# Performance work log

Measured on AMD Instinct MI355X. Metric: run time of the kernel, lower is better.

The kernel has to match this reference:

```python
import jax, jax.numpy as jnp
import numpy as np

RES = 320
B = 32

def make_trajectory():
    # Faithful to get_init_trajectory_full: grid points (i,j), zeroed inside the
    # skip bands (i in [140,170] OR j in [120,160]), then shifted by -res/2.
    I, J = np.meshgrid(np.arange(RES), np.arange(RES), indexing='ij')
    pts = np.stack([I, J], axis=-1).astype(np.float32)
    skip = ((I >= 140) & (I <= 170)) | ((J >= 120) & (J <= 160))
    pts[skip] = 0.0
    pts = pts.reshape(-1, 2) - 0.5 * RES
    return jnp.asarray(pts)

def setup_inputs():
    key = jax.random.key(0)
    k_space_input = jax.random.normal(key, (B, 1, RES, RES, 2), dtype=jnp.float32)
    trajectory = make_trajectory()
    return {"k_space_input": k_space_input, "trajectory": trajectory}

def _forward(k_space_input, trajectory):
    H = W = RES
    b = k_space_input.shape[0]
    # [B,1,H,W,2] -> permute(0,1,4,2,3).squeeze(1) -> [B,2,H,W]
    ksp = jnp.transpose(k_space_input[:, 0], (0, 3, 1, 2))
    c = ksp[:, 0] + 1j * ksp[:, 1]                       # [B,H,W] complex k-space

    # --- bilinear grid-sample at trajectory points (zero padding, align_corners=False) ---
    g = trajectory * (2.0 / W)                           # normalize [-res/2,res/2] -> [-1,1]
    x = ((g[:, 0] + 1.0) * W - 1.0) * 0.5                # pixel x (width)
    y = ((g[:, 1] + 1.0) * H - 1.0) * 0.5                # pixel y (height)
    x0f = jnp.floor(x); y0f = jnp.floor(y)
    fx = x - x0f; fy = y - y0f
    x0 = x0f.astype(jnp.int32); y0 = y0f.astype(jnp.int32)
    corners = ((x0,     y0,     (1 - fx) * (1 - fy)),
               (x0 + 1, y0,     fx       * (1 - fy)),
               (x0,     y0 + 1, (1 - fx) * fy),
               (x0 + 1, y0 + 1, fx       * fy))

    def gather(ix, iy):
        valid = (ix >= 0) & (ix < W) & (iy >= 0) & (iy < H)
        v = c[:, jnp.clip(iy, 0, H - 1), jnp.clip(ix, 0, W - 1)]   # [B,N]
        return jnp.where(valid[None, :], v, 0.0)

    sub = sum(gather(ix, iy) * w[None, :] for ix, iy, w in corners)  # [B,N] sampled k-space

    # --- NUFFT adjoint: bilinear gridding (adjoint scatter-add) + centered inverse FFT ---
    grid = jnp.zeros((b, H * W), dtype=sub.dtype)
    for ix, iy, w in corners:
        valid = (ix >= 0) & (ix < W) & (iy >= 0) & (iy < H)
        idx = jnp.clip(iy, 0, H - 1) * W + jnp.clip(ix, 0, W - 1)
        grid = grid.at[:, idx].add(sub * jnp.where(valid, w, 0.0)[None, :])
    kgrid = grid.reshape(b, H, W)
    img = jnp.fft.fftshift(
        jnp.fft.ifft2(jnp.fft.ifftshift(kgrid, axes=(-2, -1)), axes=(-2, -1)),
        axes=(-2, -1)) * (H * W)                          # adjoint DFT = N * centered ifft
    out = jnp.stack([img.real, img.imag], axis=1)         # [B,2,H,W]
    return out[:, None]                                   # unsqueeze(1) -> [B,1,2,H,W]

def reference(k_space_input, trajectory):
    return _forward(k_space_input, trajectory)
```

## Files before the change

### kernel.cpp

```cpp
#include <hip/hip_runtime.h>

#define RES 320
#define CELLS (RES * RES)
#define MDIM 640
#define NCOLS 10240
#define UF 192

#define DEGC 1360.625f

typedef __attribute__((ext_vector_type(8))) short short8;
typedef __attribute__((ext_vector_type(4))) float f32x4;

static __device__ __forceinline__ short f2bf(float f) {
    unsigned u = __builtin_bit_cast(unsigned, f);
    unsigned r = (u + 0x7fffu + ((u >> 16) & 1u)) >> 16;
    return (short)r;
}

#define GLD16(g, l) __builtin_amdgcn_global_load_lds(                        \
    (const __attribute__((address_space(1))) void*)(g),                      \
    (__attribute__((address_space(3))) void*)(l), 16, 0, 0)

__global__ __launch_bounds__(256) void stencil_mt(const float2* __restrict__ ksp,
                                                  short* __restrict__ B1t,
                                                  float* __restrict__ g00,
                                                  short* __restrict__ Ff) {
    __shared__ float2 Ls[32][33];
    int tid = threadIdx.x;

    if (blockIdx.x < 240) {
        int idx0 = (blockIdx.x * 256 + tid) * 2;
        int row = idx0 / RES, y0 = idx0 % RES;
        int isfi = row >= UF;
        int u = row - UF * isfi;
        unsigned pk = 0;
        if (u <= 160) {
#pragma unroll
            for (int h = 0; h < 2; h++) {
                int y = y0 + h;
                int rr = (u * y) % RES;
                float s, c;
                sincospif((float)rr * (2.0f / RES), &s, &c);
                float sign = ((u + y) & 1) ? -1.0f : 1.0f;
                float val = isfi ? sign * s : sign * c;
                pk |= ((unsigned)(unsigned short)f2bf(val)) << (16 * h);
            }
        }
        *(unsigned*)(Ff + idx0) = pk;
    }

    int d = blockIdx.x;
    int xcd = d & 7, r = d >> 3;
    int bb = xcd * 4 + r / 100;
    int tile = r % 100;
    int tx0 = (tile % 10) * 32, ty0 = (tile / 10) * 32;
    int xl = tid & 31, yq = tid >> 5;
    int xc = tid >> 3, yg = tid & 7;
    const float2* kb = ksp + (size_t)bb * CELLS;

    int x = tx0 + xl;
    int ax = (x < 140 || x > 170) ? 1 : 0;
    int axp = (x <= 318 && (x + 1 < 140 || x + 1 > 170)) ? 1 : 0;
    float Axs[3] = {(x >= 1) ? (float)ax : 0.f, (float)(ax + axp), (float)axp};

#pragma unroll
    for (int rr = 0; rr < 4; rr++) {
        int yl = yq + 8 * rr;
        int y = ty0 + yl;
        int by = (y < 120 || y > 160) ? 1 : 0;
        int byp = (y <= 318 && (y + 1 < 120 || y + 1 > 160)) ? 1 : 0;
        float Bys[3] = {(y >= 1) ? (float)by : 0.f, (float)(by + byp), (float)byp};

        float re = 0.f, im = 0.f;
#pragma unroll
        for (int s = 0; s < 9; s++) {
            int dy = s / 3 - 1, dx = s % 3 - 1;
            float w = 0.0625f * Axs[s % 3] * Bys[s / 3];
            int yn = min(max(y + dy, 0), RES - 1);
            int xn = min(max(x + dx, 0), RES - 1);
            float2 v = kb[yn * RES + xn];
            re = fmaf(w, v.x, re);
            im = fmaf(w, v.y, im);
        }
        if ((y | x) == 0) {
            float2 v0 = kb[0];
            re = fmaf(DEGC, v0.x, re);
            im = fmaf(DEGC, v0.y, im);
            g00[2 * bb] = re;
            g00[2 * bb + 1] = im;
            re = 0.f;
            im = 0.f;
        }
        Ls[yl][xl] = make_float2(re, im);
    }
    __syncthreads();
    float2 v0 = Ls[yg * 4 + 0][xc], v1 = Ls[yg * 4 + 1][xc];
    float2 v2 = Ls[yg * 4 + 2][xc], v3 = Ls[yg * 4 + 3][xc];
    uint2 pr, pi;
    pr.x = (unsigned short)f2bf(v0.x) | ((unsigned)(unsigned short)f2bf(v1.x) << 16);
    pr.y = (unsigned short)f2bf(v2.x) | ((unsigned)(unsigned short)f2bf(v3.x) << 16);
    pi.x = (unsigned short)f2bf(v0.y) | ((unsigned)(unsigned short)f2bf(v1.y) << 16);
    pi.y = (unsigned short)f2bf(v2.y) | ((unsigned)(unsigned short)f2bf(v3.y) << 16);
    size_t rowbase = ((size_t)bb * RES + tx0 + xc) * MDIM;
    *(uint2*)(B1t + rowbase + ty0 + yg * 4) = pr;
    *(uint2*)(B1t + rowbase + RES + ty0 + yg * 4) = pi;
}

__global__ __launch_bounds__(256) void gemm1(const short* __restrict__ Ff,
                                             const short* __restrict__ B1t,
                                             short* __restrict__ C1) {
    __shared__ __align__(16) union {
        struct { short At[2][128 * 32]; short Bt[2][128 * 32]; } s;
        float Q[2][64 * 64];
    } sm;
    int tid = threadIdx.x;
    int lane = tid & 63, wave = tid >> 6;
    int wr = wave >> 1, wc = wave & 1;
    int n0c = blockIdx.x * 64;
    int u0 = blockIdx.y * 64;
    int q = lane >> 4, tl = lane & 15;
    int row4 = tid >> 2, ko = (tid & 3) * 8;
    f32x4 acc[4][4];
#pragma unroll
    for (int i = 0; i < 4; i++)
#pragma unroll
        for (int j = 0; j < 4; j++) acc[i][j] = {0.f, 0.f, 0.f, 0.f};

#define STG1(buf, k0)                                                        \
    {                                                                        \
        GLD16(Ff + (size_t)(u0 + row4) * RES + (k0) + ko,                    \
              sm.s.At[buf] + (size_t)(wave * 64) * 8);                       \
        GLD16(Ff + (size_t)(UF + u0 + row4) * RES + (k0) + ko,               \
              sm.s.At[buf] + (size_t)(256 + wave * 64) * 8);                 \
        GLD16(B1t + (size_t)(n0c + row4) * MDIM + (k0) + ko,                 \
              sm.s.Bt[buf] + (size_t)(wave * 64) * 8);                       \
        GLD16(B1t + (size_t)(n0c + row4) * MDIM + RES + (k0) + ko,           \
              sm.s.Bt[buf] + (size_t)(256 + wave * 64) * 8);                 \
    }

    STG1(0, 0);
    __syncthreads();
    int cur = 0;
    for (int kt = 0; kt < 10; kt++) {
        if (kt < 9) STG1(cur ^ 1, (kt + 1) * 32);
        short8 a[4], bf[4];
#pragma unroll
        for (int i = 0; i < 4; i++)
            a[i] = *(const short8*)&sm.s.At[cur][(wr * 64 + i * 16 + tl) * 32 + q * 8];
#pragma unroll
        for (int j = 0; j < 4; j++)
            bf[j] = *(const short8*)&sm.s.Bt[cur][(wc * 64 + j * 16 + tl) * 32 + q * 8];
#pragma unroll
        for (int i = 0; i < 4; i++)
#pragma unroll
            for (int j = 0; j < 4; j++)
                acc[i][j] = __builtin_amdgcn_mfma_f32_16x16x32_bf16(a[i], bf[j], acc[i][j], 0, 0, 0);
        __syncthreads();
        cur ^= 1;
    }
    if (wave == 1 || wave == 3) {
        float* dst = sm.Q[wave >> 1];
#pragma unroll
        for (int i = 0; i < 4; i++)
#pragma unroll
            for (int j = 0; j < 4; j++)
#pragma unroll
                for (int t = 0; t < 4; t++)
                    dst[(i * 16 + q * 4 + t) * 64 + j * 16 + tl] = acc[i][j][t];
    }
    __syncthreads();
    if (wave == 0) {
#pragma unroll
        for (int i = 0; i < 4; i++)
#pragma unroll
            for (int j = 0; j < 4; j++)
#pragma unroll
                for (int t = 0; t < 4; t++) {
                    int r = i * 16 + q * 4 + t, cl = j * 16 + tl;
                    int u = u0 + r, col = n0c + cl;
                    float q22 = sm.Q[1][r * 64 + cl];
                    if (u <= 160)
                        C1[(size_t)u * NCOLS + col] = f2bf(acc[i][j][t] - q22);
                    if (u >= 1 && u <= 159)
                        C1[(size_t)(RES - u) * NCOLS + col] = f2bf(acc[i][j][t] + q22);
                }
    } else if (wave == 2) {
#pragma unroll
        for (int i = 0; i < 4; i++)
#pragma unroll
            for (int j = 0; j < 4; j++)
#pragma unroll
                for (int t = 0; t < 4; t++) {
                    int r = i * 16 + q * 4 + t, cl = j * 16 + tl;
                    int u = u0 + r, col = n0c + cl;
                    float q12 = sm.Q[0][r * 64 + cl];
                    if (u <= 160)
                        C1[(size_t)(RES + u) * NCOLS + col] = f2bf(q12 + acc[i][j][t]);
                    if (u >= 1 && u <= 159)
                        C1[(size_t)(2 * RES - u) * NCOLS + col] = f2bf(q12 - acc[i][j][t]);
                }
    }
}

__global__ __launch_bounds__(256) void gemm2(const short* __restrict__ C1,
                                             const short* __restrict__ Ff,
                                             const float* __restrict__ g00,
                                             float* __restrict__ out) {
    __shared__ __align__(16) union {
        struct { short At[2][128 * 32]; short Bt[2][128 * 32]; } s;
        float Q[2][64 * 64];
    } sm;
    int tid = threadIdx.x;
    int lane = tid & 63, wave = tid >> 6;
    int wr = wave >> 1, wc = wave & 1;
    int bu0 = blockIdx.x * 64;
    int n0 = blockIdx.y * 64;
    int q = lane >> 4, tl = lane & 15;
    int row4 = tid >> 2, ko = (tid & 3) * 8;
    f32x4 acc[4][4];
#pragma unroll
    for (int i = 0; i < 4; i++)
#pragma unroll
        for (int j = 0; j < 4; j++) acc[i][j] = {0.f, 0.f, 0.f, 0.f};

    int gr_s = bu0 + row4;
    unsigned bb_s = (unsigned)gr_s / 320u;
    int m_s = gr_s - (int)bb_s * 320;

#define STG2(buf, k0)                                                        \
    {                                                                        \
        GLD16(C1 + (size_t)m_s * NCOLS + bb_s * RES + (k0) + ko,             \
              sm.s.At[buf] + (size_t)(wave * 64) * 8);                       \
        GLD16(C1 + (size_t)(RES + m_s) * NCOLS + bb_s * RES + (k0) + ko,     \
              sm.s.At[buf] + (size_t)(256 + wave * 64) * 8);                 \
        GLD16(Ff + (size_t)(n0 + row4) * RES + (k0) + ko,                    \
              sm.s.Bt[buf] + (size_t)(wave * 64) * 8);                       \
        GLD16(Ff + (size_t)(UF + n0 + row4) * RES + (k0) + ko,               \
              sm.s.Bt[buf] + (size_t)(256 + wave * 64) * 8);                 \
    }

    STG2(0, 0);
    __syncthreads();
    int cur = 0;
    for (int kt = 0; kt < 10; kt++) {
        if (kt < 9) STG2(cur ^ 1, (kt + 1) * 32);
        short8 a[4], bf[4];
#pragma unroll
        for (int i = 0; i < 4; i++)
            a[i] = *(const short8*)&sm.s.At[cur][(wr * 64 + i * 16 + tl) * 32 + q * 8];
#pragma unroll
        for (int j = 0; j < 4; j++)
            bf[j] = *(const short8*)&sm.s.Bt[cur][(wc * 64 + j * 16 + tl) * 32 + q * 8];
#pragma unroll
        for (int i = 0; i < 4; i++)
#pragma unroll
            for (int j = 0; j < 4; j++)
                acc[i][j] = __builtin_amdgcn_mfma_f32_16x16x32_bf16(a[i], bf[j], acc[i][j], 0, 0, 0);
        __syncthreads();
        cur ^= 1;
    }
    if (wave == 1 || wave == 3) {
        float* dst = sm.Q[wave >> 1];
#pragma unroll
        for (int i = 0; i < 4; i++)
#pragma unroll
            for (int j = 0; j < 4; j++)
#pragma unroll
                for (int t = 0; t < 4; t++)
                    dst[(i * 16 + q * 4 + t) * 64 + j * 16 + tl] = acc[i][j][t];
    }
    __syncthreads();
    if (wave == 0) {
#pragma unroll
        for (int i = 0; i < 4; i++)
#pragma unroll
            for (int j = 0; j < 4; j++)
#pragma unroll
                for (int t = 0; t < 4; t++) {
                    int r = i * 16 + q * 4 + t, cl = j * 16 + tl;
                    int gr = bu0 + r;
                    unsigned bb = (unsigned)gr / 320u;
                    int m = gr - (int)bb * 320;
                    int np = n0 + cl;
                    float q2 = sm.Q[1][r * 64 + cl];
                    float g = g00[2 * bb];
                    float sgn = ((m + np) & 1) ? -1.0f : 1.0f;
                    size_t rowb = ((size_t)bb * 2 * RES + m) * RES;
                    if (np <= 160)
                        out[rowb + np] = (acc[i][j][t] - q2) + sgn * g;
                    if (np >= 1 && np <= 159)
                        out[rowb + (RES - np)] = (acc[i][j][t] + q2) + sgn * g;
                }
    } else if (wave == 2) {
#pragma unroll
        for (int i = 0; i < 4; i++)
#pragma unroll
            for (int j = 0; j < 4; j++)
#pragma unroll
                for (int t = 0; t < 4; t++) {
                    int r = i * 16 + q * 4 + t, cl = j * 16 + tl;
                    int gr = bu0 + r;
                    unsigned bb = (unsigned)gr / 320u;
                    int m = gr - (int)bb * 320;
                    int np = n0 + cl;
                    float q3 = sm.Q[0][r * 64 + cl];
                    float g = g00[2 * bb + 1];
                    float sgn = ((m + np) & 1) ? -1.0f : 1.0f;
                    size_t rowb = (((size_t)bb * 2 + 1) * RES + m) * RES;
                    if (np <= 160)
                        out[rowb + np] = (q3 + acc[i][j][t]) + sgn * g;
                    if (np >= 1 && np <= 159)
                        out[rowb + (RES - np)] = (acc[i][j][t] - q3) + sgn * g;
                }
    }
}

extern "C" void kernel_launch(void* const* d_in, const int* in_sizes, int n_in,
                              void* d_out, int out_size, void* d_ws, size_t ws_size,
                              hipStream_t stream) {
    const float* ksp = (const float*)d_in[0];

    short* Ff = (short*)d_ws;
    short* B1t = Ff + (size_t)2 * UF * RES;
    short* C1 = B1t + (size_t)NCOLS * MDIM;
    float* g00 = (float*)(C1 + (size_t)MDIM * NCOLS);

    stencil_mt<<<3200, 256, 0, stream>>>((const float2*)ksp, B1t, g00, Ff);
    gemm1<<<dim3(160, 3), 256, 0, stream>>>(Ff, B1t, C1);
    gemm2<<<dim3(160, 3), 256, 0, stream>>>(C1, Ff, g00, (float*)d_out);
}
```

Baseline: 114.5 us.

## Fold separable stencil into DFT matrices and read raw k-space in gemm1

The 3x3 separable gridding stencil is folded algebraically into the DFT twiddle matrices (FB along one axis, FA along the other), so the separate stencil pass and its B1t intermediate disappear. gemm1 now loads raw float2 k-space directly, converting it to bf16 in registers and writing it to padded LDS, and overlaps those loads with the MFMA work. The DC correction is computed in the gemm2 epilogue straight from the input. This cuts a full read/write pass over the batch, but gemm1 now uses register-staged loads instead of direct-to-LDS loads, and the stencil weights are rounded to bf16 inside the matrices.

```diff
diff --git a/kernel.cpp b/kernel.cpp
--- a/kernel.cpp
+++ b/kernel.cpp
@@ -21,140 +21,111 @@
     (const __attribute__((address_space(1))) void*)(g),                      \
     (__attribute__((address_space(3))) void*)(l), 16, 0, 0)
 
-__global__ __launch_bounds__(256) void stencil_mt(const float2* __restrict__ ksp,
-                                                  short* __restrict__ B1t,
-                                                  float* __restrict__ g00,
-                                                  short* __restrict__ Ff) {
-    __shared__ float2 Ls[32][33];
-    int tid = threadIdx.x;
-
-    if (blockIdx.x < 240) {
-        int idx0 = (blockIdx.x * 256 + tid) * 2;
-        int row = idx0 / RES, y0 = idx0 % RES;
-        int isfi = row >= UF;
-        int u = row - UF * isfi;
-        unsigned pk = 0;
-        if (u <= 160) {
-#pragma unroll
-            for (int h = 0; h < 2; h++) {
-                int y = y0 + h;
-                int rr = (u * y) % RES;
-                float s, c;
-                sincospif((float)rr * (2.0f / RES), &s, &c);
-                float sign = ((u + y) & 1) ? -1.0f : 1.0f;
-                float val = isfi ? sign * s : sign * c;
-                pk |= ((unsigned)(unsigned short)f2bf(val)) << (16 * h);
+__global__ __launch_bounds__(256) void gen_fafb(short* __restrict__ FBf,
+                                                short* __restrict__ FAf) {
+    int idx = blockIdx.x * 256 + threadIdx.x;
+    int mat = idx / (2 * UF * RES);
+    int r = idx - mat * (2 * UF * RES);
+    int row = r / RES, c = r % RES;
+    int plane = row >= UF;
+    int n = row - UF * plane;
+    float vr = 0.f;
+    if (n <= 160) {
+        int lo = mat ? 120 : 140, hi = mat ? 160 : 170;
+#pragma unroll
+        for (int dx = -1; dx <= 1; dx++) {
+            int xx = c - dx;
+            if (xx < 0 || xx > RES - 1) continue;
+            int a0 = (xx < lo || xx > hi) ? 1 : 0;
+            int a1 = (xx + 1 <= RES - 1 && (xx + 1 < lo || xx + 1 > hi)) ? 1 : 0;
+            float w;
+            if (dx == -1) w = (xx >= 1) ? (float)a0 : 0.f;
+            else if (dx == 0) w = (float)(a0 + ((xx <= RES - 2) ? a1 : 0));
+            else w = (xx <= RES - 2) ? (float)a1 : 0.f;
+            if (w != 0.f) {
+                int rr = (n * xx) % RES;
+                float s, cc;
+                sincospif((float)rr * (2.0f / RES), &s, &cc);
+                float sign = ((n + xx) & 1) ? -1.0f : 1.0f;
+                vr += w * sign * (plane ? s : cc);
             }
         }
-        *(unsigned*)(Ff + idx0) = pk;
-    }
-
-    int d = blockIdx.x;
-    int xcd = d & 7, r = d >> 3;
-    int bb = xcd * 4 + r / 100;
-    int tile = r % 100;
-    int tx0 = (tile % 10) * 32, ty0 = (tile / 10) * 32;
-    int xl = tid & 31, yq = tid >> 5;
-    int xc = tid >> 3, yg = tid & 7;
-    const float2* kb = ksp + (size_t)bb * CELLS;
-
-    int x = tx0 + xl;
-    int ax = (x < 140 || x > 170) ? 1 : 0;
-    int axp = (x <= 318 && (x + 1 < 140 || x + 1 > 170)) ? 1 : 0;
-    float Axs[3] = {(x >= 1) ? (float)ax : 0.f, (float)(ax + axp), (float)axp};
-
-#pragma unroll
-    for (int rr = 0; rr < 4; rr++) {
-        int yl = yq + 8 * rr;
-        int y = ty0 + yl;
-        int by = (y < 120 || y > 160) ? 1 : 0;
-        int byp = (y <= 318 && (y + 1 < 120 || y + 1 > 160)) ? 1 : 0;
-        float Bys[3] = {(y >= 1) ? (float)by : 0.f, (float)(by + byp), (float)byp};
-
-        float re = 0.f, im = 0.f;
-#pragma unroll
-        for (int s = 0; s < 9; s++) {
-            int dy = s / 3 - 1, dx = s % 3 - 1;
-            float w = 0.0625f * Axs[s % 3] * Bys[s / 3];
-            int yn = min(max(y + dy, 0), RES - 1);
-            int xn = min(max(x + dx, 0), RES - 1);
-            float2 v = kb[yn * RES + xn];
-            re = fmaf(w, v.x, re);
-            im = fmaf(w, v.y, im);
-        }
-        if ((y | x) == 0) {
-            float2 v0 = kb[0];
-            re = fmaf(DEGC, v0.x, re);
-            im = fmaf(DEGC, v0.y, im);
-            g00[2 * bb] = re;
-            g00[2 * bb + 1] = im;
-            re = 0.f;
-            im = 0.f;
-        }
-        Ls[yl][xl] = make_float2(re, im);
-    }
-    __syncthreads();
-    float2 v0 = Ls[yg * 4 + 0][xc], v1 = Ls[yg * 4 + 1][xc];
-    float2 v2 = Ls[yg * 4 + 2][xc], v3 = Ls[yg * 4 + 3][xc];
-    uint2 pr, pi;
-    pr.x = (unsigned short)f2bf(v0.x) | ((unsigned)(unsigned short)f2bf(v1.x) << 16);
-    pr.y = (unsigned short)f2bf(v2.x) | ((unsigned)(unsigned short)f2bf(v3.x) << 16);
-    pi.x = (unsigned short)f2bf(v0.y) | ((unsigned)(unsigned short)f2bf(v1.y) << 16);
-    pi.y = (unsigned short)f2bf(v2.y) | ((unsigned)(unsigned short)f2bf(v3.y) << 16);
-    size_t rowbase = ((size_t)bb * RES + tx0 + xc) * MDIM;
-    *(uint2*)(B1t + rowbase + ty0 + yg * 4) = pr;
-    *(uint2*)(B1t + rowbase + RES + ty0 + yg * 4) = pi;
-}
-
-__global__ __launch_bounds__(256) void gemm1(const short* __restrict__ Ff,
-                                             const short* __restrict__ B1t,
-                                             short* __restrict__ C1) {
+        if (mat == 0) vr *= 0.0625f;
+    }
+    (mat ? FAf : FBf)[r] = f2bf(vr);
+}
+
+__global__ __launch_bounds__(256) void gemm1(const short* __restrict__ FBf,
+                                             const float2* __restrict__ ksp,
+                                             short* __restrict__ T) {
     __shared__ __align__(16) union {
-        struct { short At[2][128 * 32]; short Bt[2][128 * 32]; } s;
+        struct { short At[2][128 * 32]; short Bt[2][128 * 40]; } s;
         float Q[2][64 * 64];
     } sm;
     int tid = threadIdx.x;
     int lane = tid & 63, wave = tid >> 6;
     int wr = wave >> 1, wc = wave & 1;
-    int n0c = blockIdx.x * 64;
-    int u0 = blockIdx.y * 64;
+    int c0 = blockIdx.x * 64;
+    int v0 = blockIdx.y * 64;
+    int b = c0 / RES, y0b = c0 % RES;
+    const float2* kb = ksp + (size_t)b * CELLS;
     int q = lane >> 4, tl = lane & 15;
     int row4 = tid >> 2, ko = (tid & 3) * 8;
+    int brow = tid >> 2, bxq = (tid & 3) * 8;
     f32x4 acc[4][4];
 #pragma unroll
     for (int i = 0; i < 4; i++)
 #pragma unroll
         for (int j = 0; j < 4; j++) acc[i][j] = {0.f, 0.f, 0.f, 0.f};
 
-#define STG1(buf, k0)                                                        \
-    {                                                                        \
-        GLD16(Ff + (size_t)(u0 + row4) * RES + (k0) + ko,                    \
+#define S1A(buf, k0)                                                         \
+    {                                                                        \
+        GLD16(FBf + (size_t)(v0 + row4) * RES + (k0) + ko,                   \
               sm.s.At[buf] + (size_t)(wave * 64) * 8);                       \
-        GLD16(Ff + (size_t)(UF + u0 + row4) * RES + (k0) + ko,               \
+        GLD16(FBf + (size_t)(UF + v0 + row4) * RES + (k0) + ko,              \
               sm.s.At[buf] + (size_t)(256 + wave * 64) * 8);                 \
-        GLD16(B1t + (size_t)(n0c + row4) * MDIM + (k0) + ko,                 \
-              sm.s.Bt[buf] + (size_t)(wave * 64) * 8);                       \
-        GLD16(B1t + (size_t)(n0c + row4) * MDIM + RES + (k0) + ko,           \
-              sm.s.Bt[buf] + (size_t)(256 + wave * 64) * 8);                 \
-    }
-
-    STG1(0, 0);
+    }
+
+    float2 bv[8];
+#define S1BLOAD(k0)                                                          \
+    {                                                                        \
+        const float2* src = kb + (size_t)(y0b + brow) * RES + (k0) + bxq;    \
+        _Pragma("unroll") for (int e = 0; e < 8; e++) bv[e] = src[e];        \
+    }
+#define S1BWRITE(buf)                                                        \
+    {                                                                        \
+        short8 r8, i8;                                                       \
+        _Pragma("unroll") for (int e = 0; e < 8; e++) {                      \
+            r8[e] = f2bf(bv[e].x);                                           \
+            i8[e] = f2bf(bv[e].y);                                           \
+        }                                                                    \
+        *(short8*)&sm.s.Bt[buf][brow * 40 + bxq] = r8;                       \
+        *(short8*)&sm.s.Bt[buf][(64 + brow) * 40 + bxq] = i8;                \
+    }
+
+    S1A(0, 0);
+    S1BLOAD(0);
+    S1BWRITE(0);
     __syncthreads();
     int cur = 0;
     for (int kt = 0; kt < 10; kt++) {
-        if (kt < 9) STG1(cur ^ 1, (kt + 1) * 32);
+        if (kt < 9) {
+            S1A(cur ^ 1, (kt + 1) * 32);
+            S1BLOAD((kt + 1) * 32);
+        }
         short8 a[4], bf[4];
 #pragma unroll
         for (int i = 0; i < 4; i++)
             a[i] = *(const short8*)&sm.s.At[cur][(wr * 64 + i * 16 + tl) * 32 + q * 8];
 #pragma unroll
         for (int j = 0; j < 4; j++)
-            bf[j] = *(const short8*)&sm.s.Bt[cur][(wc * 64 + j * 16 + tl) * 32 + q * 8];
+            bf[j] = *(const short8*)&sm.s.Bt[cur][(wc * 64 + j * 16 + tl) * 40 + q * 8];
 #pragma unroll
         for (int i = 0; i < 4; i++)
 #pragma unroll
             for (int j = 0; j < 4; j++)
                 acc[i][j] = __builtin_amdgcn_mfma_f32_16x16x32_bf16(a[i], bf[j], acc[i][j], 0, 0, 0);
+        if (kt < 9) S1BWRITE(cur ^ 1);
         __syncthreads();
         cur ^= 1;
     }
@@ -177,12 +148,12 @@
 #pragma unroll
                 for (int t = 0; t < 4; t++) {
                     int r = i * 16 + q * 4 + t, cl = j * 16 + tl;
-                    int u = u0 + r, col = n0c + cl;
-                    float q22 = sm.Q[1][r * 64 + cl];
-                    if (u <= 160)
-                        C1[(size_t)u * NCOLS + col] = f2bf(acc[i][j][t] - q22);
-                    if (u >= 1 && u <= 159)
-                        C1[(size_t)(RES - u) * NCOLS + col] = f2bf(acc[i][j][t] + q22);
+                    int n = v0 + r, y = y0b + cl;
+                    float q11 = sm.Q[1][r * 64 + cl];
+                    if (n <= 160)
+                        T[(size_t)(b * RES + n) * MDIM + y] = f2bf(acc[i][j][t] - q11);
+                    if (n >= 1 && n <= 159)
+                        T[(size_t)(b * RES + RES - n) * MDIM + y] = f2bf(acc[i][j][t] + q11);
                 }
     } else if (wave == 2) {
 #pragma unroll
@@ -192,19 +163,19 @@
 #pragma unroll
                 for (int t = 0; t < 4; t++) {
                     int r = i * 16 + q * 4 + t, cl = j * 16 + tl;
-                    int u = u0 + r, col = n0c + cl;
-                    float q12 = sm.Q[0][r * 64 + cl];
-                    if (u <= 160)
-                        C1[(size_t)(RES + u) * NCOLS + col] = f2bf(q12 + acc[i][j][t]);
-                    if (u >= 1 && u <= 159)
-                        C1[(size_t)(2 * RES - u) * NCOLS + col] = f2bf(q12 - acc[i][j][t]);
-                }
-    }
-}
-
-__global__ __launch_bounds__(256) void gemm2(const short* __restrict__ C1,
-                                             const short* __restrict__ Ff,
-                                             const float* __restrict__ g00,
+                    int n = v0 + r, y = y0b + cl;
+                    float q01 = sm.Q[0][r * 64 + cl];
+                    if (n <= 160)
+                        T[(size_t)(b * RES + n) * MDIM + RES + y] = f2bf(q01 + acc[i][j][t]);
+                    if (n >= 1 && n <= 159)
+                        T[(size_t)(b * RES + RES - n) * MDIM + RES + y] = f2bf(q01 - acc[i][j][t]);
+                }
+    }
+}
+
+__global__ __launch_bounds__(256) void gemm2(const short* __restrict__ T,
+                                             const short* __restrict__ FAf,
+                                             const float2* __restrict__ ksp,
                                              float* __restrict__ out) {
     __shared__ __align__(16) union {
         struct { short At[2][128 * 32]; short Bt[2][128 * 32]; } s;
@@ -213,8 +184,9 @@
     int tid = threadIdx.x;
     int lane = tid & 63, wave = tid >> 6;
     int wr = wave >> 1, wc = wave & 1;
-    int bu0 = blockIdx.x * 64;
-    int n0 = blockIdx.y * 64;
+    int c0 = blockIdx.x * 64;
+    int v0 = blockIdx.y * 64;
+    int b = c0 / RES, n0b = c0 % RES;
     int q = lane >> 4, tl = lane & 15;
     int row4 = tid >> 2, ko = (tid & 3) * 8;
     f32x4 acc[4][4];
@@ -223,27 +195,23 @@
 #pragma unroll
         for (int j = 0; j < 4; j++) acc[i][j] = {0.f, 0.f, 0.f, 0.f};
 
-    int gr_s = bu0 + row4;
-    unsigned bb_s = (unsigned)gr_s / 320u;
-    int m_s = gr_s - (int)bb_s * 320;
-
-#define STG2(buf, k0)                                                        \
-    {                                                                        \
-        GLD16(C1 + (size_t)m_s * NCOLS + bb_s * RES + (k0) + ko,             \
+#define S2(buf, k0)                                                          \
+    {                                                                        \
+        GLD16(FAf + (size_t)(v0 + row4) * RES + (k0) + ko,                   \
               sm.s.At[buf] + (size_t)(wave * 64) * 8);                       \
-        GLD16(C1 + (size_t)(RES + m_s) * NCOLS + bb_s * RES + (k0) + ko,     \
+        GLD16(FAf + (size_t)(UF + v0 + row4) * RES + (k0) + ko,              \
               sm.s.At[buf] + (size_t)(256 + wave * 64) * 8);                 \
-        GLD16(Ff + (size_t)(n0 + row4) * RES + (k0) + ko,                    \
+        GLD16(T + (size_t)(c0 + row4) * MDIM + (k0) + ko,                    \
               sm.s.Bt[buf] + (size_t)(wave * 64) * 8);                       \
-        GLD16(Ff + (size_t)(UF + n0 + row4) * RES + (k0) + ko,               \
+        GLD16(T + (size_t)(c0 + row4) * MDIM + RES + (k0) + ko,              \
               sm.s.Bt[buf] + (size_t)(256 + wave * 64) * 8);                 \
     }
 
-    STG2(0, 0);
+    S2(0, 0);
     __syncthreads();
     int cur = 0;
     for (int kt = 0; kt < 10; kt++) {
-        if (kt < 9) STG2(cur ^ 1, (kt + 1) * 32);
+        if (kt < 9) S2(cur ^ 1, (kt + 1) * 32);
         short8 a[4], bf[4];
 #pragma unroll
         for (int i = 0; i < 4; i++)
@@ -270,47 +238,42 @@
                     dst[(i * 16 + q * 4 + t) * 64 + j * 16 + tl] = acc[i][j][t];
     }
     __syncthreads();
+    float2 g0 = ksp[(size_t)b * CELLS];
     if (wave == 0) {
-#pragma unroll
-        for (int i = 0; i < 4; i++)
-#pragma unroll
-            for (int j = 0; j < 4; j++)
-#pragma unroll
-                for (int t = 0; t < 4; t++) {
-                    int r = i * 16 + q * 4 + t, cl = j * 16 + tl;
-                    int gr = bu0 + r;
-                    unsigned bb = (unsigned)gr / 320u;
-                    int m = gr - (int)bb * 320;
-                    int np = n0 + cl;
-                    float q2 = sm.Q[1][r * 64 + cl];
-                    float g = g00[2 * bb];
-                    float sgn = ((m + np) & 1) ? -1.0f : 1.0f;
-                    size_t rowb = ((size_t)bb * 2 * RES + m) * RES;
-                    if (np <= 160)
-                        out[rowb + np] = (acc[i][j][t] - q2) + sgn * g;
-                    if (np >= 1 && np <= 159)
-                        out[rowb + (RES - np)] = (acc[i][j][t] + q2) + sgn * g;
+        float g = DEGC * g0.x;
+#pragma unroll
+        for (int i = 0; i < 4; i++)
+#pragma unroll
+            for (int j = 0; j < 4; j++)
+#pragma unroll
+                for (int t = 0; t < 4; t++) {
+                    int r = i * 16 + q * 4 + t, cl = j * 16 + tl;
+                    int m = v0 + r, n = n0b + cl;
+                    float q11 = sm.Q[1][r * 64 + cl];
+                    float sgn = ((m + n) & 1) ? -1.0f : 1.0f;
+                    size_t pb = (size_t)(b * 2) * RES;
+                    if (m <= 160)
+                        out[(pb + m) * RES + n] = (acc[i][j][t] - q11) + sgn * g;
+                    if (m >= 1 && m <= 159)
+                        out[(pb + RES - m) * RES + n] = (acc[i][j][t] + q11) + sgn * g;
                 }
     } else if (wave == 2) {
-#pragma unroll
-        for (int i = 0; i < 4; i++)
-#pragma unroll
-            for (int j = 0; j < 4; j++)
-#pragma unroll
-                for (int t = 0; t < 4; t++) {
-                    int r = i * 16 + q * 4 + t, cl = j * 16 + tl;
-                    int gr = bu0 + r;
-                    unsigned bb = (unsigned)gr / 320u;
-                    int m = gr - (int)bb * 320;
-                    int np = n0 + cl;
-                    float q3 = sm.Q[0][r * 64 + cl];
-                    float g = g00[2 * bb + 1];
-                    float sgn = ((m + np) & 1) ? -1.0f : 1.0f;
-                    size_t rowb = (((size_t)bb * 2 + 1) * RES + m) * RES;
-                    if (np <= 160)
-                        out[rowb + np] = (q3 + acc[i][j][t]) + sgn * g;
-                    if (np >= 1 && np <= 159)
-                        out[rowb + (RES - np)] = (acc[i][j][t] - q3) + sgn * g;
+        float g = DEGC * g0.y;
+#pragma unroll
+        for (int i = 0; i < 4; i++)
+#pragma unroll
+            for (int j = 0; j < 4; j++)
+#pragma unroll
+                for (int t = 0; t < 4; t++) {
+                    int r = i * 16 + q * 4 + t, cl = j * 16 + tl;
+                    int m = v0 + r, n = n0b + cl;
+                    float q01 = sm.Q[0][r * 64 + cl];
+                    float sgn = ((m + n) & 1) ? -1.0f : 1.0f;
+                    size_t pb = (size_t)(b * 2 + 1) * RES;
+                    if (m <= 160)
+                        out[(pb + m) * RES + n] = (q01 + acc[i][j][t]) + sgn * g;
+                    if (m >= 1 && m <= 159)
+                        out[(pb + RES - m) * RES + n] = (q01 - acc[i][j][t]) + sgn * g;
                 }
     }
 }
@@ -318,14 +281,13 @@
 extern "C" void kernel_launch(void* const* d_in, const int* in_sizes, int n_in,
                               void* d_out, int out_size, void* d_ws, size_t ws_size,
                               hipStream_t stream) {
-    const float* ksp = (const float*)d_in[0];
-
-    short* Ff = (short*)d_ws;
-    short* B1t = Ff + (size_t)2 * UF * RES;
-    short* C1 = B1t + (size_t)NCOLS * MDIM;
-    float* g00 = (float*)(C1 + (size_t)MDIM * NCOLS);
-
-    stencil_mt<<<3200, 256, 0, stream>>>((const float2*)ksp, B1t, g00, Ff);
-    gemm1<<<dim3(160, 3), 256, 0, stream>>>(Ff, B1t, C1);
-    gemm2<<<dim3(160, 3), 256, 0, stream>>>(C1, Ff, g00, (float*)d_out);
-}
+    const float2* ksp = (const float2*)d_in[0];
+
+    short* FBf = (short*)d_ws;
+    short* FAf = FBf + (size_t)2 * UF * RES;
+    short* T = FAf + (size_t)2 * UF * RES;
+
+    gen_fafb<<<960, 256, 0, stream>>>(FBf, FAf);
+    gemm1<<<dim3(160, 3), 256, 0, stream>>>(FBf, ksp, T);
+    gemm2<<<dim3(160, 3), 256, 0, stream>>>(T, FAf, ksp, (float*)d_out);
+}
```

After: 109.4 us. -4.5%, faster.
